# Optimization experiments

Hardware: AMD Instinct MI355X
Metric: run time of the kernel (lower is better)

The kernel has to match this reference:

```python
import jax, jax.numpy as jnp
import numpy as np

N_FINE = 50000
N_COARSE = 2000
N_EDGES = 300000
HID = 512
OUT = 3
K = 3


def _gcn_prep(edge_index, n):
    # PyG GCNConv with add_self_loops=True, improved=False, edge_weight=1
    row, col = edge_index[0], edge_index[1]
    loop = jnp.arange(n, dtype=edge_index.dtype)
    row = jnp.concatenate([row, loop])
    col = jnp.concatenate([col, loop])
    deg = jax.ops.segment_sum(jnp.ones(row.shape[0], dtype=jnp.float32), col, num_segments=n)
    dis = jax.lax.rsqrt(deg)  # deg >= 1 due to self loops
    norm = dis[row] * dis[col]
    return row, col, norm


def _gcn(h, W, b, row, col, norm, n):
    # linear -> gather source -> weight by norm -> scatter-add at target -> +bias
    h = h @ W
    msg = h[row] * norm[:, None]
    return jax.ops.segment_sum(msg, col, num_segments=n) + b


def _knn_interpolate(y, coarse_pos, fine_pos, k=K):
    # squared euclidean distances [N_fine, N_coarse]
    d2 = (jnp.sum(fine_pos * fine_pos, axis=1, keepdims=True)
          + jnp.sum(coarse_pos * coarse_pos, axis=1)[None, :]
          - 2.0 * fine_pos @ coarse_pos.T)
    neg, idx = jax.lax.top_k(-d2, k)          # k nearest
    w = 1.0 / jnp.maximum(-neg, 1e-16)        # inverse squared-distance weights
    return jnp.einsum('nk,nkc->nc', w, y[idx]) / jnp.sum(w, axis=1, keepdims=True)


def setup_inputs() -> dict:
    key = jax.random.key(0)
    ks = jax.random.split(key, 20)
    x = jax.random.normal(ks[0], (N_FINE, 5), dtype=jnp.float32)
    sdf = jax.random.normal(ks[1], (N_FINE, 1), dtype=jnp.float32)
    edge_index = jax.random.randint(ks[2], (2, N_EDGES), 0, N_FINE)
    coarse_x = jax.random.normal(ks[3], (N_COARSE, 2), dtype=jnp.float32)
    coarse_y = jax.random.normal(ks[4], (N_COARSE, OUT), dtype=jnp.float32)
    dims_pre = [(6, HID), (HID, HID), (HID, HID)]
    dims_end = [(OUT + HID, HID), (HID, HID), (HID, OUT)]
    out = {"x": x, "sdf": sdf, "coarse_x": coarse_x, "coarse_y": coarse_y,
           "edge_index": edge_index}
    for i, (di, do) in enumerate(dims_pre):
        out[f"pre_W{i}"] = jax.random.normal(ks[5 + i], (di, do), dtype=jnp.float32) / np.float32(np.sqrt(di))
        out[f"pre_b{i}"] = jnp.zeros((do,), dtype=jnp.float32)
    for i, (di, do) in enumerate(dims_end):
        out[f"end_W{i}"] = jax.random.normal(ks[10 + i], (di, do), dtype=jnp.float32) / np.float32(np.sqrt(di))
        out[f"end_b{i}"] = jnp.zeros((do,), dtype=jnp.float32)
    return out


def reference(x, sdf, coarse_x, coarse_y, edge_index,
              pre_W0, pre_b0, pre_W1, pre_b1, pre_W2, pre_b2,
              end_W0, end_b0, end_W1, end_b1, end_W2, end_b2):
    n = x.shape[0]
    row, col, norm = _gcn_prep(edge_index, n)

    fine_x = jnp.concatenate([x, sdf], axis=1)  # [N, 6]
    for W, b in ((pre_W0, pre_b0), (pre_W1, pre_b1), (pre_W2, pre_b2)):
        fine_x = jax.nn.relu(_gcn(fine_x, W, b, row, col, norm, n))

    # coarse -> fine KNN upsample (batch.x[:, :2] are fine node positions)
    fine_y_orig = _knn_interpolate(coarse_y, coarse_x[:, :2], x[:, :2])  # [N, 3]

    fine_y = jnp.concatenate([fine_y_orig, fine_x], axis=1)  # [N, 515]
    for W, b in ((end_W0, end_b0), (end_W1, end_b1)):
        fine_y = jax.nn.relu(_gcn(fine_y, W, b, row, col, norm, n))
    fine_y = _gcn(fine_y, end_W2, end_b2, row, col, norm, n)
    return fine_y  # residual=False
```

## Files before the change

### kernel.cpp

```cpp
#include <hip/hip_runtime.h>
#include <hip/hip_bf16.h>

#define N_FINE 50000
#define N_COARSE 2000
#define N_EDGES 300000

typedef short  s16x8 __attribute__((ext_vector_type(8)));
typedef float  f32x4 __attribute__((ext_vector_type(4)));

static inline int cdiv(int a, int b) { return (a + b - 1) / b; }

__device__ __forceinline__ short f2b(float f) {
    unsigned u = __builtin_bit_cast(unsigned, f);
    unsigned r = (u + 0x7fffu + ((u >> 16) & 1u)) >> 16;
    return (short)r;
}
__device__ __forceinline__ float b2f(short s) {
    return __builtin_bit_cast(float, ((unsigned)(unsigned short)s) << 16);
}

#define GL16(gsrc, ldst) __builtin_amdgcn_global_load_lds( \
    (const __attribute__((address_space(1))) unsigned*)(gsrc), \
    (__attribute__((address_space(3))) unsigned*)(ldst), 16, 0, 0)


__global__ void count_edges_kernel(const int* __restrict__ col, int* __restrict__ counts, int ne) {
    int e = blockIdx.x * 256 + threadIdx.x;
    if (e < ne) atomicAdd(&counts[col[e]], 1);
}

__global__ void compute_dis_kernel(const int* __restrict__ counts, float* __restrict__ dis, int n) {
    int i = blockIdx.x * 256 + threadIdx.x;
    if (i < n) dis[i] = rsqrtf((float)(counts[i] + 1));
}

__global__ __launch_bounds__(1024) void scan_block_kernel(const int* __restrict__ counts,
        int* __restrict__ rowptr, int* __restrict__ blksum, int n) {
    __shared__ int wsum[16];
    int tid = threadIdx.x, lane = tid & 63, wv = tid >> 6;
    int i = blockIdx.x * 1024 + tid;
    int v = (i < n) ? counts[i] : 0;
    int x = v;
#pragma unroll
    for (int off = 1; off < 64; off <<= 1) {
        int t = __shfl_up(x, off);
        if (lane >= off) x += t;
    }
    if (lane == 63) wsum[wv] = x;
    __syncthreads();
    if (wv == 0) {
        int s = (lane < 16) ? wsum[lane] : 0;
#pragma unroll
        for (int off = 1; off < 16; off <<= 1) {
            int t = __shfl_up(s, off);
            if (lane >= off) s += t;
        }
        if (lane < 16) wsum[lane] = s;
    }
    __syncthreads();
    int prefix = (wv > 0) ? wsum[wv - 1] : 0;
    int incl = prefix + x;
    if (i < n) rowptr[i] = incl - v;
    if (tid == 1023) blksum[blockIdx.x] = incl;
}

__global__ void scan_tops_kernel(int* __restrict__ blksum, int nb) {
    int lane = threadIdx.x;
    int v = (lane < nb) ? blksum[lane] : 0;
    int x = v;
#pragma unroll
    for (int off = 1; off < 64; off <<= 1) {
        int t = __shfl_up(x, off);
        if (lane >= off) x += t;
    }
    if (lane < nb) blksum[lane] = x - v;
}

__global__ void scan_add_kernel(int* __restrict__ rowptr, const int* __restrict__ blksum, int n) {
    int i = blockIdx.x * 256 + threadIdx.x;
    if (i < n) rowptr[i] += blksum[i >> 10];
    else if (i == n) rowptr[n] = N_EDGES;
}

__global__ void scatter_edges_kernel(const int* __restrict__ row, const int* __restrict__ col,
                                     int* __restrict__ cursor, int* __restrict__ esrc, int ne) {
    int e = blockIdx.x * 256 + threadIdx.x;
    if (e < ne) {
        int p = atomicAdd(&cursor[col[e]], 1);
        esrc[p] = row[e];
    }
}


__global__ __launch_bounds__(256) void wt4_kernel(
        const float* __restrict__ W0, const float* __restrict__ W1,
        const float* __restrict__ W2, const float* __restrict__ W3,
        short* __restrict__ T0, short* __restrict__ T1,
        short* __restrict__ T2, short* __restrict__ T3) {
    __shared__ float tile[32][33];
    const float* W; short* WT;
    switch (blockIdx.y) {
        case 0: W = W0; WT = T0; break;
        case 1: W = W1; WT = T1; break;
        case 2: W = W2; WT = T2; break;
        default: W = W3; WT = T3; break;
    }
    int bx = blockIdx.x & 15;
    int by = blockIdx.x >> 4;
    int tx = threadIdx.x & 31;
    int ty = threadIdx.x >> 5;
#pragma unroll
    for (int i = 0; i < 4; ++i) {
        int k = bx * 32 + ty + i * 8;
        int n = by * 32 + tx;
        tile[ty + i * 8][tx] = W[(size_t)k * 512 + n];
    }
    __syncthreads();
#pragma unroll
    for (int i = 0; i < 4; ++i) {
        int n = by * 32 + ty + i * 8;
        int k = bx * 32 + tx;
        WT[(size_t)n * 512 + k] = f2b(tile[tx][ty + i * 8]);
    }
}


__global__ void pre0_kernel(const float* __restrict__ x, const float* __restrict__ sdf,
                            const float* __restrict__ W, const float* __restrict__ dis,
                            short* __restrict__ B, int M) {
    int idx = blockIdx.x * 256 + threadIdx.x;
    int m = idx >> 9, n = idx & 511;
    if (m >= M) return;
    float a0 = x[m*5+0], a1 = x[m*5+1], a2 = x[m*5+2], a3 = x[m*5+3], a4 = x[m*5+4], a5 = sdf[m];
    float t = a0*W[n] + a1*W[512+n] + a2*W[1024+n] + a3*W[1536+n] + a4*W[2048+n] + a5*W[2560+n];
    B[(size_t)m*512+n] = f2b(dis[m] * t);
}

__global__ __launch_bounds__(256) void gemm512_mfma_kernel(
        const short* __restrict__ A, const short* __restrict__ WT,
        const float* __restrict__ dis, short* __restrict__ C, int M,
        const float* __restrict__ A2, const float* __restrict__ W2) {
    __shared__ __attribute__((aligned(16))) short As[2][4096];
    __shared__ __attribute__((aligned(16))) short Bs[2][4096];
    int tid  = threadIdx.x;
    int lane = tid & 63;
    int w    = tid >> 6;
    int wr   = w >> 1, wc = w & 1;
    int row0 = blockIdx.x * 128;
    int col0 = blockIdx.y * 128;

    int rb0 = 2 * w, rb1 = 2 * w + 1;
    int rIn = lane & 15, kc = lane >> 4;
    int ar0 = row0 + rb0 * 16 + rIn; if (ar0 >= M) ar0 = M - 1;
    int ar1 = row0 + rb1 * 16 + rIn; if (ar1 >= M) ar1 = M - 1;
    const short* aSrc0 = A  + (size_t)ar0 * 512 + kc * 8;
    const short* aSrc1 = A  + (size_t)ar1 * 512 + kc * 8;
    const short* bSrc0 = WT + (size_t)(col0 + rb0 * 16 + rIn) * 512 + kc * 8;
    const short* bSrc1 = WT + (size_t)(col0 + rb1 * 16 + rIn) * 512 + kc * 8;
    int aOff0 = rb0 * 512, aOff1 = rb1 * 512;

    f32x4 acc[4][4] = {};

    auto stage = [&](int buf, int k0) {
        GL16(aSrc0 + k0, &As[buf][aOff0]);
        GL16(aSrc1 + k0, &As[buf][aOff1]);
        GL16(bSrc0 + k0, &Bs[buf][aOff0]);
        GL16(bSrc1 + k0, &Bs[buf][aOff1]);
    };
    auto compute = [&](int buf) {
        s16x8 av[4], bv[4];
#pragma unroll
        for (int mi = 0; mi < 4; ++mi) av[mi] = *(const s16x8*)&As[buf][(wr * 4 + mi) * 512 + lane * 8];
#pragma unroll
        for (int ni = 0; ni < 4; ++ni) bv[ni] = *(const s16x8*)&Bs[buf][(wc * 4 + ni) * 512 + lane * 8];
#pragma unroll
        for (int mi = 0; mi < 4; ++mi)
#pragma unroll
            for (int ni = 0; ni < 4; ++ni)
                acc[mi][ni] = __builtin_amdgcn_mfma_f32_16x16x32_bf16(av[mi], bv[ni], acc[mi][ni], 0, 0, 0);
    };

    stage(0, 0);
    __syncthreads();
#pragma unroll 1
    for (int tt = 0; tt < 8; ++tt) {
        int kA = tt * 64 + 32;
        if (kA < 512) stage(1, kA);
        compute(0);
        __syncthreads();
        int kB = tt * 64 + 64;
        if (kB < 512) stage(0, kB);
        compute(1);
        __syncthreads();
    }

    int rbase = row0 + wr * 64;
    int cbase = col0 + wc * 64;
#pragma unroll
    for (int mi = 0; mi < 4; ++mi) {
#pragma unroll
        for (int r = 0; r < 4; ++r) {
            int row = rbase + mi * 16 + (lane >> 4) * 4 + r;
            if (row >= M) continue;
            float d = dis[row];
            float a20 = 0.f, a21 = 0.f, a22 = 0.f;
            if (A2) { a20 = A2[row*3+0]; a21 = A2[row*3+1]; a22 = A2[row*3+2]; }
#pragma unroll
            for (int ni = 0; ni < 4; ++ni) {
                int col = cbase + ni * 16 + (lane & 15);
                float v = acc[mi][ni][r];
                if (A2) v += a20 * W2[col] + a21 * W2[512 + col] + a22 * W2[1024 + col];
                C[(size_t)row * 512 + col] = f2b(d * v);
            }
        }
    }
}

__global__ __launch_bounds__(256) void spmm512_kernel(
        const short* __restrict__ B, const int* __restrict__ rowptr, const int* __restrict__ esrc,
        const float* __restrict__ dis, const float* __restrict__ bias,
        short* __restrict__ out, int M) {
    int node = blockIdx.x * 4 + (threadIdx.x >> 6);
    int lane = threadIdx.x & 63;
    if (node >= M) return;
    const s16x8* Bv = (const s16x8*)B;
    s16x8 v = Bv[(size_t)node * 64 + lane];
    float acc[8];
#pragma unroll
    for (int j = 0; j < 8; ++j) acc[j] = b2f(v[j]);
    int s = rowptr[node], e = rowptr[node + 1];
    for (int p = s; p < e; ++p) {
        int src = esrc[p];
        s16x8 t = Bv[(size_t)src * 64 + lane];
#pragma unroll
        for (int j = 0; j < 8; ++j) acc[j] += b2f(t[j]);
    }
    float d = dis[node];
    const float4* bp = (const float4*)bias;
    float4 b0 = bp[lane * 2], b1 = bp[lane * 2 + 1];
    float r[8];
    r[0] = d*acc[0] + b0.x; r[1] = d*acc[1] + b0.y; r[2] = d*acc[2] + b0.z; r[3] = d*acc[3] + b0.w;
    r[4] = d*acc[4] + b1.x; r[5] = d*acc[5] + b1.y; r[6] = d*acc[6] + b1.z; r[7] = d*acc[7] + b1.w;
    s16x8 o;
#pragma unroll
    for (int j = 0; j < 8; ++j) o[j] = f2b(fmaxf(r[j], 0.f));
    ((s16x8*)out)[(size_t)node * 64 + lane] = o;
}

__global__ __launch_bounds__(256) void gemm_n3_kernel(
        const short* __restrict__ A, const float* __restrict__ W,
        const float* __restrict__ dis, float* __restrict__ B3, int M) {
    int wid = (blockIdx.x * 256 + threadIdx.x) >> 6;
    int lane = threadIdx.x & 63;
    if (wid >= M) return;
    s16x8 v = ((const s16x8*)A)[(size_t)wid * 64 + lane];
    float s0 = 0.f, s1 = 0.f, s2 = 0.f;
#pragma unroll
    for (int j = 0; j < 8; ++j) {
        float a = b2f(v[j]);
        int k = lane * 8 + j;
        s0 += a * W[k*3+0];
        s1 += a * W[k*3+1];
        s2 += a * W[k*3+2];
    }
    for (int off = 32; off > 0; off >>= 1) {
        s0 += __shfl_down(s0, off);
        s1 += __shfl_down(s1, off);
        s2 += __shfl_down(s2, off);
    }
    if (lane == 0) {
        float d = dis[wid];
        B3[wid*3+0] = d * s0;
        B3[wid*3+1] = d * s1;
        B3[wid*3+2] = d * s2;
    }
}

__global__ void spmm3_kernel(const float* __restrict__ B3, const int* __restrict__ rowptr,
                             const int* __restrict__ esrc, const float* __restrict__ dis,
                             const float* __restrict__ bias, float* __restrict__ out, int M) {
    int i = blockIdx.x * 256 + threadIdx.x;
    if (i >= M) return;
    float a0 = B3[i*3+0], a1 = B3[i*3+1], a2 = B3[i*3+2];
    int s = rowptr[i], e = rowptr[i + 1];
    for (int p = s; p < e; ++p) {
        int src = esrc[p];
        a0 += B3[src*3+0];
        a1 += B3[src*3+1];
        a2 += B3[src*3+2];
    }
    float d = dis[i];
    out[i*3+0] = d * a0 + bias[0];
    out[i*3+1] = d * a1 + bias[1];
    out[i*3+2] = d * a2 + bias[2];
}

__global__ __launch_bounds__(256) void knn_kernel(
        const float* __restrict__ x, const float* __restrict__ cpos,
        const float* __restrict__ cy, float* __restrict__ fy, int M) {
    __shared__ float sd[12][64];
    __shared__ int   si[12][64];
    int lane = threadIdx.x & 63;
    int w = threadIdx.x >> 6;
    int gi = blockIdx.x * 64 + lane;
    int i = (gi < M) ? gi : (M - 1);
    float px = x[i*5+0], py = x[i*5+1];
    float pn2 = px*px + py*py;
    float d0 = 3.0e38f, d1 = 3.0e38f, d2 = 3.0e38f;
    int i0 = 0x7fffffff, i1 = 0x7fffffff, i2 = 0x7fffffff;
    int c0 = w * (N_COARSE / 4), c1 = c0 + (N_COARSE / 4);
    for (int c = c0; c < c1; ++c) {
        float a = cpos[c*2+0], b = cpos[c*2+1];
        float sn2 = a*a + b*b;
        float d = pn2 + sn2 - 2.f * (px * a + py * b);
        if (d < d2) {
            if (d < d1) {
                d2 = d1; i2 = i1;
                if (d < d0) { d1 = d0; i1 = i0; d0 = d; i0 = c; }
                else       { d1 = d;  i1 = c; }
            } else { d2 = d; i2 = c; }
        }
    }
    sd[w*3+0][lane] = d0; si[w*3+0][lane] = i0;
    sd[w*3+1][lane] = d1; si[w*3+1][lane] = i1;
    sd[w*3+2][lane] = d2; si[w*3+2][lane] = i2;
    __syncthreads();
    if (w != 0 || gi >= M) return;
    float cd[12]; int ci[12];
#pragma unroll
    for (int q = 0; q < 12; ++q) { cd[q] = sd[q][lane]; ci[q] = si[q][lane]; }
    float bd[3]; int bi[3];
#pragma unroll
    for (int s = 0; s < 3; ++s) {
        float best = 3.4e38f; int besti = 0x7fffffff; int bq = 0;
#pragma unroll
        for (int q = 0; q < 12; ++q) {
            bool better = (cd[q] < best) || (cd[q] == best && ci[q] < besti);
            if (better) { best = cd[q]; besti = ci[q]; bq = q; }
        }
        bd[s] = best; bi[s] = besti;
        cd[bq] = 3.4e38f; ci[bq] = 0x7fffffff;
    }
    float w0 = 1.f / fmaxf(bd[0], 1e-16f);
    float w1 = 1.f / fmaxf(bd[1], 1e-16f);
    float w2 = 1.f / fmaxf(bd[2], 1e-16f);
    float ws = w0 + w1 + w2;
    int j0 = bi[0], j1 = bi[1], j2 = bi[2];
#pragma unroll
    for (int j = 0; j < 3; ++j) {
        float v = w0 * cy[j0*3+j] + w1 * cy[j1*3+j] + w2 * cy[j2*3+j];
        fy[gi*3+j] = v / ws;
    }
}


extern "C" void kernel_launch(void* const* d_in, const int* in_sizes, int n_in,
                              void* d_out, int out_size, void* d_ws, size_t ws_size,
                              hipStream_t stream) {
    const float* x        = (const float*)d_in[0];
    const float* sdf      = (const float*)d_in[1];
    const float* coarse_x = (const float*)d_in[2];
    const float* coarse_y = (const float*)d_in[3];
    const int*   eidx     = (const int*)d_in[4];
    const float* pre_W0   = (const float*)d_in[5];
    const float* pre_b0   = (const float*)d_in[6];
    const float* pre_W1   = (const float*)d_in[7];
    const float* pre_b1   = (const float*)d_in[8];
    const float* pre_W2   = (const float*)d_in[9];
    const float* pre_b2   = (const float*)d_in[10];
    const float* end_W0   = (const float*)d_in[11];
    const float* end_b0   = (const float*)d_in[12];
    const float* end_W1   = (const float*)d_in[13];
    const float* end_b1   = (const float*)d_in[14];
    const float* end_W2   = (const float*)d_in[15];
    const float* end_b2   = (const float*)d_in[16];
    float* out = (float*)d_out;

    const int M = N_FINE, NE = N_EDGES;
    const int* erow = eidx;
    const int* ecol = eidx + NE;

    char* base = (char*)d_ws;
    size_t off = 0;
    auto alloc = [&](size_t bytes) { char* p = base + off; off = (off + bytes + 255) & ~(size_t)255; return p; };
    int*   counts = (int*)  alloc((size_t)M * 4);
    int*   rowptr = (int*)  alloc((size_t)(M + 1) * 4);
    int*   cursor = (int*)  alloc((size_t)M * 4);
    int*   esrc   = (int*)  alloc((size_t)NE * 4);
    int*   blksum = (int*)  alloc((size_t)64 * 4);
    float* dis    = (float*)alloc((size_t)M * 4);
    float* fy     = (float*)alloc((size_t)M * 3 * 4);
    float* B3     = (float*)alloc((size_t)M * 3 * 4);
    short* WT1    = (short*)alloc((size_t)512 * 512 * 2);
    short* WT2    = (short*)alloc((size_t)512 * 512 * 2);
    short* WT3    = (short*)alloc((size_t)512 * 512 * 2);
    short* WT4    = (short*)alloc((size_t)512 * 512 * 2);
    short* bufA   = (short*)alloc((size_t)M * 512 * 2);
    short* bufB   = (short*)alloc((size_t)M * 512 * 2);
    (void)ws_size;

    wt4_kernel<<<dim3(256, 4), 256, 0, stream>>>(pre_W1, pre_W2, end_W0 + 3 * 512, end_W1,
                                                 WT1, WT2, WT3, WT4);

    hipMemsetAsync(counts, 0, (size_t)M * 4, stream);
    count_edges_kernel<<<cdiv(NE, 256), 256, 0, stream>>>(ecol, counts, NE);
    compute_dis_kernel<<<cdiv(M, 256), 256, 0, stream>>>(counts, dis, M);
    int nb = cdiv(M, 1024);
    scan_block_kernel<<<nb, 1024, 0, stream>>>(counts, rowptr, blksum, M);
    scan_tops_kernel<<<1, 64, 0, stream>>>(blksum, nb);
    scan_add_kernel<<<cdiv(M + 1, 256), 256, 0, stream>>>(rowptr, blksum, M);
    hipMemcpyAsync(cursor, rowptr, (size_t)M * 4, hipMemcpyDeviceToDevice, stream);
    scatter_edges_kernel<<<cdiv(NE, 256), 256, 0, stream>>>(erow, ecol, cursor, esrc, NE);

    knn_kernel<<<cdiv(M, 64), 256, 0, stream>>>(x, coarse_x, coarse_y, fy, M);

    dim3 ggrid(cdiv(M, 128), 4);
    int sgrid = cdiv(M, 4);

    pre0_kernel<<<cdiv(M * 512, 256), 256, 0, stream>>>(x, sdf, pre_W0, dis, bufB, M);
    spmm512_kernel<<<sgrid, 256, 0, stream>>>(bufB, rowptr, esrc, dis, pre_b0, bufA, M);

    gemm512_mfma_kernel<<<ggrid, 256, 0, stream>>>(bufA, WT1, dis, bufB, M, nullptr, nullptr);
    spmm512_kernel<<<sgrid, 256, 0, stream>>>(bufB, rowptr, esrc, dis, pre_b1, bufA, M);

    gemm512_mfma_kernel<<<ggrid, 256, 0, stream>>>(bufA, WT2, dis, bufB, M, nullptr, nullptr);
    spmm512_kernel<<<sgrid, 256, 0, stream>>>(bufB, rowptr, esrc, dis, pre_b2, bufA, M);

    gemm512_mfma_kernel<<<ggrid, 256, 0, stream>>>(bufA, WT3, dis, bufB, M, fy, end_W0);
    spmm512_kernel<<<sgrid, 256, 0, stream>>>(bufB, rowptr, esrc, dis, end_b0, bufA, M);

    gemm512_mfma_kernel<<<ggrid, 256, 0, stream>>>(bufA, WT4, dis, bufB, M, nullptr, nullptr);
    spmm512_kernel<<<sgrid, 256, 0, stream>>>(bufB, rowptr, esrc, dis, end_b1, bufA, M);

    gemm_n3_kernel<<<cdiv(M * 64, 256), 256, 0, stream>>>(bufA, end_W2, dis, B3, M);
    spmm3_kernel<<<cdiv(M, 256), 256, 0, stream>>>(B3, rowptr, esrc, dis, end_b2, out, M);
}
```

Measured before the change: 822.0 us.

## Double GEMM K-tile depth and remap blocks into grouped 1D grid

The 512-wide MFMA GEMM now stages 64-deep K slices per buffer instead of 32, which halves the number of barrier-separated pipeline iterations and doubles LDS use per block. The 2D grid becomes a 1D grid remapped so that groups of 8 row tiles cover all 4 column tiles consecutively, which is meant to improve L2 reuse of A rows. The larger LDS footprint may reduce occupancy, and blocks past the last row tile exit early.

```diff
diff --git a/kernel.cpp b/kernel.cpp
--- a/kernel.cpp
+++ b/kernel.cpp
@@ -140,14 +140,20 @@
         const short* __restrict__ A, const short* __restrict__ WT,
         const float* __restrict__ dis, short* __restrict__ C, int M,
         const float* __restrict__ A2, const float* __restrict__ W2) {
-    __shared__ __attribute__((aligned(16))) short As[2][4096];
-    __shared__ __attribute__((aligned(16))) short Bs[2][4096];
+    __shared__ __attribute__((aligned(16))) short As[2][8192];
+    __shared__ __attribute__((aligned(16))) short Bs[2][8192];
     int tid  = threadIdx.x;
     int lane = tid & 63;
     int w    = tid >> 6;
     int wr   = w >> 1, wc = w & 1;
-    int row0 = blockIdx.x * 128;
-    int col0 = blockIdx.y * 128;
+
+    int nbx = (M + 127) >> 7;
+    int id = blockIdx.x;
+    int bx = ((id >> 5) << 3) | (id & 7);
+    int by = (id >> 3) & 3;
+    if (bx >= nbx) return;
+    int row0 = bx * 128;
+    int col0 = by * 128;
 
     int rb0 = 2 * w, rb1 = 2 * w + 1;
     int rIn = lane & 15, kc = lane >> 4;
@@ -157,38 +163,47 @@
     const short* aSrc1 = A  + (size_t)ar1 * 512 + kc * 8;
     const short* bSrc0 = WT + (size_t)(col0 + rb0 * 16 + rIn) * 512 + kc * 8;
     const short* bSrc1 = WT + (size_t)(col0 + rb1 * 16 + rIn) * 512 + kc * 8;
-    int aOff0 = rb0 * 512, aOff1 = rb1 * 512;
+    int o0 = rb0 * 512, o1 = rb1 * 512;
 
     f32x4 acc[4][4] = {};
 
     auto stage = [&](int buf, int k0) {
-        GL16(aSrc0 + k0, &As[buf][aOff0]);
-        GL16(aSrc1 + k0, &As[buf][aOff1]);
-        GL16(bSrc0 + k0, &Bs[buf][aOff0]);
-        GL16(bSrc1 + k0, &Bs[buf][aOff1]);
+        GL16(aSrc0 + k0,      &As[buf][o0]);
+        GL16(aSrc1 + k0,      &As[buf][o1]);
+        GL16(bSrc0 + k0,      &Bs[buf][o0]);
+        GL16(bSrc1 + k0,      &Bs[buf][o1]);
+        GL16(aSrc0 + k0 + 32, &As[buf][4096 + o0]);
+        GL16(aSrc1 + k0 + 32, &As[buf][4096 + o1]);
+        GL16(bSrc0 + k0 + 32, &Bs[buf][4096 + o0]);
+        GL16(bSrc1 + k0 + 32, &Bs[buf][4096 + o1]);
     };
     auto compute = [&](int buf) {
-        s16x8 av[4], bv[4];
-#pragma unroll
-        for (int mi = 0; mi < 4; ++mi) av[mi] = *(const s16x8*)&As[buf][(wr * 4 + mi) * 512 + lane * 8];
-#pragma unroll
-        for (int ni = 0; ni < 4; ++ni) bv[ni] = *(const s16x8*)&Bs[buf][(wc * 4 + ni) * 512 + lane * 8];
-#pragma unroll
-        for (int mi = 0; mi < 4; ++mi)
+#pragma unroll
+        for (int s = 0; s < 2; ++s) {
+            s16x8 av[4], bv[4];
+#pragma unroll
+            for (int mi = 0; mi < 4; ++mi)
+                av[mi] = *(const s16x8*)&As[buf][s * 4096 + (wr * 4 + mi) * 512 + lane * 8];
 #pragma unroll
             for (int ni = 0; ni < 4; ++ni)
-                acc[mi][ni] = __builtin_amdgcn_mfma_f32_16x16x32_bf16(av[mi], bv[ni], acc[mi][ni], 0, 0, 0);
+                bv[ni] = *(const s16x8*)&Bs[buf][s * 4096 + (wc * 4 + ni) * 512 + lane * 8];
+#pragma unroll
+            for (int mi = 0; mi < 4; ++mi)
+#pragma unroll
+                for (int ni = 0; ni < 4; ++ni)
+                    acc[mi][ni] = __builtin_amdgcn_mfma_f32_16x16x32_bf16(av[mi], bv[ni], acc[mi][ni], 0, 0, 0);
+        }
     };
 
     stage(0, 0);
     __syncthreads();
 #pragma unroll 1
-    for (int tt = 0; tt < 8; ++tt) {
-        int kA = tt * 64 + 32;
+    for (int tt = 0; tt < 4; ++tt) {
+        int kA = tt * 128 + 64;
         if (kA < 512) stage(1, kA);
         compute(0);
         __syncthreads();
-        int kB = tt * 64 + 64;
+        int kB = tt * 128 + 128;
         if (kB < 512) stage(0, kB);
         compute(1);
         __syncthreads();
@@ -414,7 +429,8 @@
 
     knn_kernel<<<cdiv(M, 64), 256, 0, stream>>>(x, coarse_x, coarse_y, fy, M);
 
-    dim3 ggrid(cdiv(M, 128), 4);
+    int nbx = cdiv(M, 128);
+    int ggrid = cdiv(nbx, 8) * 32;
     int sgrid = cdiv(M, 4);
 
     pre0_kernel<<<cdiv(M * 512, 256), 256, 0, stream>>>(x, sdf, pre_W0, dis, bufB, M);
```

Result: slower. 852.8 us (+3.7%).
